# Optimization experiments

Hardware: AMD Instinct MI355X
Metric: run time of the kernel (lower is better)

The kernel has to match this reference:

```python
import jax, jax.numpy as jnp
import numpy as np

B, T, F = 8192, 50, 24
H1, LAT, H3 = 64, 32, 64  # encoder LSTM1, bottleneck LSTM2, decoder LSTM3


def lstm(x, W, U, b, return_sequences):
    """Keras LSTM with activation='relu', recurrent_activation='sigmoid'.
    x: [B, T, D]; W: [D, 4H]; U: [H, 4H]; b: [4H]. Gate order: i, f, g(c), o.
    """
    H = U.shape[0]
    xW = jnp.einsum('btd,dh->bth', x, W) + b          # precompute input projections
    xW_t = jnp.swapaxes(xW, 0, 1)                     # [T, B, 4H]
    h0 = jnp.zeros((x.shape[0], H), x.dtype)
    c0 = jnp.zeros((x.shape[0], H), x.dtype)

    def step(carry, xt):
        h, c = carry
        z = xt + h @ U                                 # [B, 4H]
        i = jax.nn.sigmoid(z[:, 0 * H:1 * H])
        f = jax.nn.sigmoid(z[:, 1 * H:2 * H])
        g = jax.nn.relu(z[:, 2 * H:3 * H])             # activation='relu'
        o = jax.nn.sigmoid(z[:, 3 * H:4 * H])
        c_new = f * c + i * g
        h_new = o * jax.nn.relu(c_new)                 # activation='relu'
        return (h_new, c_new), h_new

    (h_T, _), hs = jax.lax.scan(step, (h0, c0), xW_t)
    if return_sequences:
        return jnp.swapaxes(hs, 0, 1)                  # [B, T, H]
    return h_T                                         # [B, H]


def setup_inputs() -> dict:
    key = jax.random.key(0)
    ks = jax.random.split(key, 12)
    s = 0.05
    return {
        'x':  jax.random.normal(ks[0], (B, T, F), jnp.float32),
        'W1': jax.random.normal(ks[1], (F, 4 * H1), jnp.float32) * s,
        'U1': jax.random.normal(ks[2], (H1, 4 * H1), jnp.float32) * s,
        'b1': jnp.zeros((4 * H1,), jnp.float32),
        'W2': jax.random.normal(ks[3], (H1, 4 * LAT), jnp.float32) * s,
        'U2': jax.random.normal(ks[4], (LAT, 4 * LAT), jnp.float32) * s,
        'b2': jnp.zeros((4 * LAT,), jnp.float32),
        'W3': jax.random.normal(ks[5], (LAT, 4 * H3), jnp.float32) * s,
        'U3': jax.random.normal(ks[6], (H3, 4 * H3), jnp.float32) * s,
        'b3': jnp.zeros((4 * H3,), jnp.float32),
        'Wd': jax.random.normal(ks[7], (H3, F), jnp.float32) * s,
        'bd': jnp.zeros((F,), jnp.float32),
    }


def reference(x, W1, U1, b1, W2, U2, b2, W3, U3, b3, Wd, bd):
    # Encoder
    h1 = lstm(x, W1, U1, b1, return_sequences=True)    # [B, T, 64]
    z = lstm(h1, W2, U2, b2, return_sequences=False)   # [B, latent]
    # Decoder
    zr = jnp.broadcast_to(z[:, None, :], (z.shape[0], T, z.shape[1]))  # RepeatVector
    h3 = lstm(zr, W3, U3, b3, return_sequences=True)   # [B, T, 64]
    out = jnp.einsum('bth,hf->btf', h3, Wd) + bd       # TimeDistributed Dense
    return out
```

## Files before the change

### kernel.cpp

```cpp
#include <hip/hip_runtime.h>
#include <cstdint>

#define BB 8192
#define TT 50
#define FF 24
#define ROWS 32
#define LOG2E 1.4426950408889634f

typedef __attribute__((ext_vector_type(8))) short short8;
typedef __attribute__((ext_vector_type(4))) float f32x4;

__device__ __forceinline__ float sig2(float xs){
  return __builtin_amdgcn_rcpf(1.0f + __builtin_amdgcn_exp2f(-xs));
}

__device__ __forceinline__ unsigned cvtpk(float a, float b){
  unsigned r;
  asm("v_cvt_pk_bf16_f32 %0, %1, %2" : "=v"(r) : "v"(a), "v"(b));
  return r;
}

__device__ __forceinline__ unsigned short rne16(float v){
  unsigned b = __float_as_uint(v);
  b += 0x7FFFu + ((b >> 16) & 1u);
  return (unsigned short)(b >> 16);
}

__device__ __forceinline__ void phase_barrier(){
  asm volatile("s_waitcnt lgkmcnt(0)" ::: "memory");
  __builtin_amdgcn_s_barrier();
  asm volatile("" ::: "memory");
}

#define MFMA(A,B,C) __builtin_amdgcn_mfma_f32_16x16x32_bf16((A),(B),(C),0,0,0)


__global__ __launch_bounds__(1024,4)
void ae_fused(
    const float* __restrict__ x,
    const float* __restrict__ W1, const float* __restrict__ U1, const float* __restrict__ b1,
    const float* __restrict__ W2, const float* __restrict__ U2, const float* __restrict__ b2,
    const float* __restrict__ W3, const float* __restrict__ U3, const float* __restrict__ b3,
    const float* __restrict__ Wd, const float* __restrict__ bd,
    float* __restrict__ out)
{
  constexpr int AS1 = 104, AS2 = 40, AS3 = 72;
  __shared__ __align__(16) unsigned short a1[2][ROWS*AS1];
  __shared__ __align__(16) unsigned short a2[2][ROWS*AS2];
  __shared__ __align__(16) unsigned short a3[2][ROWS*AS3];

  const int tid = threadIdx.x, wave = tid>>6, lane = tid&63;
  const int quad = lane>>4, li = lane&15;
  const int w7 = wave&7, rg = wave>>3;
  const int b0 = blockIdx.x*ROWS;
  const int arow = rg*16 + li;

  const int gl = li & 3;
  const float scl = (gl==2) ? 1.0f : LOG2E;

  short8 A1w[2][3];
  f32x4 bi1[2];
#pragma unroll
  for (int tp=0; tp<2; ++tp){
    const int zc = gl*64 + 8*w7 + 2*(li>>2) + tp;
#pragma unroll
    for (int ks=0; ks<3; ++ks){
      short8 v1;
#pragma unroll
      for (int j=0; j<8; ++j){
        const int kk = quad*8 + j;
        float w;
        if (ks < 2) w = U1[(ks*32+kk)*256+zc];
        else        w = (kk<24) ? W1[kk*256+zc] : 0.f;
        v1[j] = (short)rne16(w*scl);
      }
      A1w[tp][ks]=v1;
    }
#pragma unroll
    for (int i2=0;i2<4;++i2)
      bi1[tp][i2] = b1[i2*64 + 8*w7 + 2*quad + tp] * ((i2==2)?1.0f:LOG2E);
  }
  short8 A1w2[3];
  f32x4 bi2;
  {
    const int zc = gl*32 + 4*w7 + (li>>2);
#pragma unroll
    for (int ks=0; ks<3; ++ks){
      short8 v1;
#pragma unroll
      for (int j=0; j<8; ++j){
        const int kk = quad*8 + j;
        float w = (ks<2) ? W2[(ks*32+kk)*128+zc] : U2[kk*128+zc];
        v1[j] = (short)rne16(w*scl);
      }
      A1w2[ks]=v1;
    }
#pragma unroll
    for (int i2=0;i2<4;++i2)
      bi2[i2] = b2[i2*32 + 4*w7 + quad] * ((i2==2)?1.0f:LOG2E);
  }

  { unsigned* p1 = (unsigned*)a1; for (int i=tid;i<2*ROWS*AS1/2;i+=1024) p1[i]=0u;
    unsigned* p2 = (unsigned*)a2; for (int i=tid;i<2*ROWS*AS2/2;i+=1024) p2[i]=0u;
    unsigned* p3 = (unsigned*)a3; for (int i=tid;i<2*ROWS*AS3/2;i+=1024) p3[i]=0u; }
  __syncthreads();
  if (tid < ROWS*FF){
    const int r = tid/FF, f = tid - r*FF;
    a1[0][r*AS1 + 64 + f] = rne16(x[((size_t)(b0+r)*TT + 0)*FF + f]);
  }
  int pr=0, pf=0; const float* xp=nullptr;
  float va=0.f, vb=0.f;
  const bool st = (tid < ROWS*FF);
  if (st){
    pr = tid/FF; pf = tid - pr*FF;
    xp = x + (size_t)(b0+pr)*TT*FF + pf;
    va = xp[1*FF];
    vb = xp[2*FF];
  }
  float c1s[2] = {0.f,0.f};
  float c2s = 0.f;
  const int rb1 = arow*AS1;
  const int rb2 = arow*AS2;
  const int hw1p = rb1 + 8*w7 + 2*quad;
  const int hw2 = rb2 + 4*w7 + quad;
  __syncthreads();

#pragma unroll 1
  for (int t=0; t<=TT; ++t){
    const int s = t&1, ns = s^1;
    float vc = 0.f;
    if (st && t+3 < TT) vc = xp[(t+3)*FF];
    short8 Bh0 = *(const short8*)&a1[s][rb1 +      quad*8];
    short8 Bh1 = *(const short8*)&a1[s][rb1 + 32 + quad*8];
    if (t < TT){
      short8 Bx = *(const short8*)&a1[s][rb1 + 64 + quad*8];
      float hp[2];
#pragma unroll
      for (int tp=0; tp<2; ++tp){
        f32x4 C = bi1[tp];
        C = MFMA(A1w[tp][0], Bh0, C);
        C = MFMA(A1w[tp][1], Bh1, C);
        C = MFMA(A1w[tp][2], Bx,  C);
        const float ig = sig2(C[0]), fg = sig2(C[1]);
        const float gg = fmaxf(C[2],0.f), og = sig2(C[3]);
        const float cn = fg*c1s[tp] + ig*gg; c1s[tp] = cn;
        hp[tp] = og*fmaxf(cn,0.f);
      }
      *(unsigned*)&a1[ns][hw1p] = cvtpk(hp[0], hp[1]);
    }
    if (t >= 1){
      f32x4 C = bi2;
      C = MFMA(A1w2[0], Bh0, C);
      C = MFMA(A1w2[1], Bh1, C);
      {
        short8 Bh2 = *(const short8*)&a2[s][rb2 + quad*8];
        C = MFMA(A1w2[2], Bh2, C);
      }
      const float ig = sig2(C[0]), fg = sig2(C[1]);
      const float gg = fmaxf(C[2],0.f), og = sig2(C[3]);
      const float cn = fg*c2s + ig*gg; c2s = cn;
      const float h = og*fmaxf(cn,0.f);
      a2[ns][hw2] = (unsigned short)cvtpk(h, h);
    }
    if (st && t < TT-1){
      a1[ns][pr*AS1 + 64 + pf] = (unsigned short)cvtpk(va, va);
      va = vb; vb = vc;
    }
    phase_barrier();
  }

  short8 A1u[2][2];
  short8 A1w3[2];
  f32x4 bi3[2];
#pragma unroll
  for (int tp=0; tp<2; ++tp){
    const int zc = gl*64 + 8*w7 + 2*(li>>2) + tp;
#pragma unroll
    for (int ks=0; ks<2; ++ks){
      short8 v1;
#pragma unroll
      for (int j=0; j<8; ++j){
        const int k = ks*32 + quad*8 + j;
        v1[j] = (short)rne16(U3[k*256+zc]*scl);
      }
      A1u[tp][ks]=v1;
    }
    {
      short8 v1;
#pragma unroll
      for (int j=0; j<8; ++j){
        const int k = quad*8 + j;
        v1[j] = (short)rne16(W3[k*256+zc]*scl);
      }
      A1w3[tp]=v1;
    }
#pragma unroll
    for (int i2=0;i2<4;++i2)
      bi3[tp][i2] = b3[i2*64 + 8*w7 + 2*quad + tp] * ((i2==2)?1.0f:LOG2E);
  }
  const bool dW = (w7 < 2);
  const int dcol = w7*16 + li;
  const bool dOK = dW && (dcol < 24);
  const float bdv = dOK ? bd[dcol] : 0.f;
  short8 Bd1[2];
  if (dW){
#pragma unroll
    for (int ks=0; ks<2; ++ks){
      short8 v1;
#pragma unroll
      for (int j=0; j<8; ++j){
        const int k = ks*32 + quad*8 + j;
        v1[j] = (short)rne16(dOK ? Wd[k*24+dcol] : 0.f);
      }
      Bd1[ks]=v1;
    }
  }

  f32x4 zr[2];
  {
    short8 Ba = *(const short8*)&a2[1][rb2 + quad*8];
#pragma unroll
    for (int tp=0; tp<2; ++tp){
      f32x4 C = bi3[tp];
      C = MFMA(A1w3[tp], Ba, C);
      zr[tp] = C;
    }
  }
  float c3s[2] = {0.f,0.f};
  const int rb3 = arow*AS3;
  const int hw3p = rb3 + 8*w7 + 2*quad;

#pragma unroll 1
  for (int t=0; t<=TT; ++t){
    const int s = t&1, ns = s^1;
    if (t < TT){
      short8 Ba[2];
#pragma unroll
      for (int ks=0; ks<2; ++ks)
        Ba[ks] = *(const short8*)&a3[s][rb3 + ks*32 + quad*8];
      float hp[2];
#pragma unroll
      for (int tp=0; tp<2; ++tp){
        f32x4 C = zr[tp];
        C = MFMA(A1u[tp][0], Ba[0], C);
        C = MFMA(A1u[tp][1], Ba[1], C);
        const float ig = sig2(C[0]), fg = sig2(C[1]);
        const float gg = fmaxf(C[2],0.f), og = sig2(C[3]);
        const float cn = fg*c3s[tp] + ig*gg; c3s[tp] = cn;
        hp[tp] = og*fmaxf(cn,0.f);
      }
      *(unsigned*)&a3[ns][hw3p] = cvtpk(hp[0], hp[1]);
      if (dW && t > 0){
        f32x4 Cd = {bdv,bdv,bdv,bdv};
        Cd = MFMA(Ba[0], Bd1[0], Cd);
        Cd = MFMA(Ba[1], Bd1[1], Cd);
        if (dcol < 24){
#pragma unroll
          for (int i2=0;i2<4;++i2)
            out[((size_t)(b0+rg*16+quad*4+i2)*TT + (t-1))*FF + dcol] = Cd[i2];
        }
      }
    } else {
      if (dW){
        f32x4 Cd = {bdv,bdv,bdv,bdv};
#pragma unroll
        for (int ks=0; ks<2; ++ks){
          short8 Ba = *(const short8*)&a3[s][rb3 + ks*32 + quad*8];
          Cd = MFMA(Ba, Bd1[ks], Cd);
        }
        if (dcol < 24){
#pragma unroll
          for (int i2=0;i2<4;++i2)
            out[((size_t)(b0+rg*16+quad*4+i2)*TT + (TT-1))*FF + dcol] = Cd[i2];
        }
      }
    }
    phase_barrier();
  }
}

extern "C" void kernel_launch(void* const* d_in, const int* in_sizes, int n_in,
                              void* d_out, int out_size, void* d_ws, size_t ws_size,
                              hipStream_t stream){
  const float* x  = (const float*)d_in[0];
  const float* W1 = (const float*)d_in[1];
  const float* U1 = (const float*)d_in[2];
  const float* b1 = (const float*)d_in[3];
  const float* W2 = (const float*)d_in[4];
  const float* U2 = (const float*)d_in[5];
  const float* b2 = (const float*)d_in[6];
  const float* W3 = (const float*)d_in[7];
  const float* U3 = (const float*)d_in[8];
  const float* b3 = (const float*)d_in[9];
  const float* Wd = (const float*)d_in[10];
  const float* bd = (const float*)d_in[11];
  float* out = (float*)d_out;

  hipLaunchKernelGGL(ae_fused, dim3(BB/ROWS), dim3(1024), 0, stream,
                     x, W1, U1, b1, W2, U2, b2, W3, U3, b3, Wd, bd, out);
}
```

Baseline: 191.0 us.

## Stagger MFMA and gate phases across row groups to overlap matrix and VALU work

Each recurrent loop is split into half-steps. The two row-group halves of the block alternate, so one half issues MFMAs while the other evaluates the gate nonlinearities, with a barrier after every half-step. The aim is to keep both the matrix units and the vector ALUs busy instead of running them one after the other in every wave. In exchange the number of block-wide barriers roughly doubles, and accumulator results must be carried across phases in registers.

```diff
diff --git a/kernel.cpp b/kernel.cpp
--- a/kernel.cpp
+++ b/kernel.cpp
@@ -125,46 +125,70 @@
   const int hw2 = rb2 + 4*w7 + quad;
   __syncthreads();
 
+  f32x4 Cl1a, Cl1b, Cl2;
 #pragma unroll 1
-  for (int t=0; t<=TT; ++t){
-    const int s = t&1, ns = s^1;
-    float vc = 0.f;
-    if (st && t+3 < TT) vc = xp[(t+3)*FF];
-    short8 Bh0 = *(const short8*)&a1[s][rb1 +      quad*8];
-    short8 Bh1 = *(const short8*)&a1[s][rb1 + 32 + quad*8];
-    if (t < TT){
-      short8 Bx = *(const short8*)&a1[s][rb1 + 64 + quad*8];
-      float hp[2];
-#pragma unroll
-      for (int tp=0; tp<2; ++tp){
-        f32x4 C = bi1[tp];
-        C = MFMA(A1w[tp][0], Bh0, C);
-        C = MFMA(A1w[tp][1], Bh1, C);
-        C = MFMA(A1w[tp][2], Bx,  C);
-        const float ig = sig2(C[0]), fg = sig2(C[1]);
-        const float gg = fmaxf(C[2],0.f), og = sig2(C[3]);
-        const float cn = fg*c1s[tp] + ig*gg; c1s[tp] = cn;
-        hp[tp] = og*fmaxf(cn,0.f);
-      }
-      *(unsigned*)&a1[ns][hw1p] = cvtpk(hp[0], hp[1]);
-    }
-    if (t >= 1){
-      f32x4 C = bi2;
-      C = MFMA(A1w2[0], Bh0, C);
-      C = MFMA(A1w2[1], Bh1, C);
-      {
-        short8 Bh2 = *(const short8*)&a2[s][rb2 + quad*8];
-        C = MFMA(A1w2[2], Bh2, C);
-      }
-      const float ig = sig2(C[0]), fg = sig2(C[1]);
-      const float gg = fmaxf(C[2],0.f), og = sig2(C[3]);
-      const float cn = fg*c2s + ig*gg; c2s = cn;
-      const float h = og*fmaxf(cn,0.f);
-      a2[ns][hw2] = (unsigned short)cvtpk(h, h);
-    }
-    if (st && t < TT-1){
-      a1[ns][pr*AS1 + 64 + pf] = (unsigned short)cvtpk(va, va);
-      va = vb; vb = vc;
+  for (int p = 0; p <= 2*TT+2; ++p){
+    if (((p ^ rg) & 1) == 0){
+      const int mt = (p - rg) >> 1;
+      if (mt <= TT){
+        const int s = mt & 1;
+        short8 Bh0 = *(const short8*)&a1[s][rb1 +      quad*8];
+        short8 Bh1 = *(const short8*)&a1[s][rb1 + 32 + quad*8];
+        if (mt < TT){
+          short8 Bx = *(const short8*)&a1[s][rb1 + 64 + quad*8];
+          { f32x4 C = bi1[0];
+            C = MFMA(A1w[0][0], Bh0, C);
+            C = MFMA(A1w[0][1], Bh1, C);
+            C = MFMA(A1w[0][2], Bx,  C); Cl1a = C; }
+          { f32x4 C = bi1[1];
+            C = MFMA(A1w[1][0], Bh0, C);
+            C = MFMA(A1w[1][1], Bh1, C);
+            C = MFMA(A1w[1][2], Bx,  C); Cl1b = C; }
+        }
+        if (mt >= 1){
+          f32x4 C = bi2;
+          C = MFMA(A1w2[0], Bh0, C);
+          C = MFMA(A1w2[1], Bh1, C);
+          short8 Bh2 = *(const short8*)&a2[s][rb2 + quad*8];
+          C = MFMA(A1w2[2], Bh2, C);
+          Cl2 = C;
+        }
+      }
+    } else {
+      const int gt = (p - rg - 1) >> 1;
+      if (gt >= 0 && gt <= TT){
+        const int ns = (gt & 1) ^ 1;
+        if (gt < TT){
+          float hp[2];
+          { f32x4 C = Cl1a;
+            const float ig = sig2(C[0]), fg = sig2(C[1]);
+            const float gg = fmaxf(C[2],0.f), og = sig2(C[3]);
+            const float cn = fg*c1s[0] + ig*gg; c1s[0] = cn;
+            hp[0] = og*fmaxf(cn,0.f); }
+          { f32x4 C = Cl1b;
+            const float ig = sig2(C[0]), fg = sig2(C[1]);
+            const float gg = fmaxf(C[2],0.f), og = sig2(C[3]);
+            const float cn = fg*c1s[1] + ig*gg; c1s[1] = cn;
+            hp[1] = og*fmaxf(cn,0.f); }
+          *(unsigned*)&a1[ns][hw1p] = cvtpk(hp[0], hp[1]);
+        }
+        if (gt >= 1){
+          f32x4 C = Cl2;
+          const float ig = sig2(C[0]), fg = sig2(C[1]);
+          const float gg = fmaxf(C[2],0.f), og = sig2(C[3]);
+          const float cn = fg*c2s + ig*gg; c2s = cn;
+          const float h = og*fmaxf(cn,0.f);
+          a2[ns][hw2] = (unsigned short)cvtpk(h, h);
+        }
+      }
+    }
+    if (((p & 1) == 0) && st){
+      const int tx = (p >> 1) + 1;
+      if (tx < TT){
+        a1[tx&1][pr*AS1 + 64 + pf] = (unsigned short)cvtpk(va, va);
+        va = vb;
+        if (tx+2 < TT) vb = xp[(tx+2)*FF];
+      }
     }
     phase_barrier();
   }
@@ -229,50 +253,52 @@
   float c3s[2] = {0.f,0.f};
   const int rb3 = arow*AS3;
   const int hw3p = rb3 + 8*w7 + 2*quad;
-
+  __syncthreads();
+
+  f32x4 Cl3a, Cl3b;
 #pragma unroll 1
-  for (int t=0; t<=TT; ++t){
-    const int s = t&1, ns = s^1;
-    if (t < TT){
-      short8 Ba[2];
-#pragma unroll
-      for (int ks=0; ks<2; ++ks)
-        Ba[ks] = *(const short8*)&a3[s][rb3 + ks*32 + quad*8];
-      float hp[2];
-#pragma unroll
-      for (int tp=0; tp<2; ++tp){
-        f32x4 C = zr[tp];
-        C = MFMA(A1u[tp][0], Ba[0], C);
-        C = MFMA(A1u[tp][1], Ba[1], C);
-        const float ig = sig2(C[0]), fg = sig2(C[1]);
-        const float gg = fmaxf(C[2],0.f), og = sig2(C[3]);
-        const float cn = fg*c3s[tp] + ig*gg; c3s[tp] = cn;
-        hp[tp] = og*fmaxf(cn,0.f);
-      }
-      *(unsigned*)&a3[ns][hw3p] = cvtpk(hp[0], hp[1]);
-      if (dW && t > 0){
-        f32x4 Cd = {bdv,bdv,bdv,bdv};
-        Cd = MFMA(Ba[0], Bd1[0], Cd);
-        Cd = MFMA(Ba[1], Bd1[1], Cd);
-        if (dcol < 24){
-#pragma unroll
-          for (int i2=0;i2<4;++i2)
-            out[((size_t)(b0+rg*16+quad*4+i2)*TT + (t-1))*FF + dcol] = Cd[i2];
+  for (int p = 0; p <= 2*TT+1; ++p){
+    if (((p ^ rg) & 1) == 0){
+      const int mt = (p - rg) >> 1;
+      if (mt <= TT){
+        const int s = mt & 1;
+        short8 Ba0 = *(const short8*)&a3[s][rb3 +      quad*8];
+        short8 Ba1 = *(const short8*)&a3[s][rb3 + 32 + quad*8];
+        if (mt < TT){
+          { f32x4 C = zr[0];
+            C = MFMA(A1u[0][0], Ba0, C);
+            C = MFMA(A1u[0][1], Ba1, C); Cl3a = C; }
+          { f32x4 C = zr[1];
+            C = MFMA(A1u[1][0], Ba0, C);
+            C = MFMA(A1u[1][1], Ba1, C); Cl3b = C; }
+        }
+        if (dW && mt > 0){
+          f32x4 Cd = {bdv,bdv,bdv,bdv};
+          Cd = MFMA(Ba0, Bd1[0], Cd);
+          Cd = MFMA(Ba1, Bd1[1], Cd);
+          if (dcol < 24){
+#pragma unroll
+            for (int i2=0;i2<4;++i2)
+              out[((size_t)(b0+rg*16+quad*4+i2)*TT + (mt-1))*FF + dcol] = Cd[i2];
+          }
         }
       }
     } else {
-      if (dW){
-        f32x4 Cd = {bdv,bdv,bdv,bdv};
-#pragma unroll
-        for (int ks=0; ks<2; ++ks){
-          short8 Ba = *(const short8*)&a3[s][rb3 + ks*32 + quad*8];
-          Cd = MFMA(Ba, Bd1[ks], Cd);
-        }
-        if (dcol < 24){
-#pragma unroll
-          for (int i2=0;i2<4;++i2)
-            out[((size_t)(b0+rg*16+quad*4+i2)*TT + (TT-1))*FF + dcol] = Cd[i2];
-        }
+      const int gt = (p - rg - 1) >> 1;
+      if (gt >= 0 && gt < TT){
+        const int ns = (gt & 1) ^ 1;
+        float hp[2];
+        { f32x4 C = Cl3a;
+          const float ig = sig2(C[0]), fg = sig2(C[1]);
+          const float gg = fmaxf(C[2],0.f), og = sig2(C[3]);
+          const float cn = fg*c3s[0] + ig*gg; c3s[0] = cn;
+          hp[0] = og*fmaxf(cn,0.f); }
+        { f32x4 C = Cl3b;
+          const float ig = sig2(C[0]), fg = sig2(C[1]);
+          const float gg = fmaxf(C[2],0.f), og = sig2(C[3]);
+          const float cn = fg*c3s[1] + ig*gg; c3s[1] = cn;
+          hp[1] = og*fmaxf(cn,0.f); }
+        *(unsigned*)&a3[ns][hw3p] = cvtpk(hp[0], hp[1]);
       }
     }
     phase_barrier();
```

New measurement: 229.1 us. +20.0%, slower.
